# Kernel optimization log

Measured on AMD Instinct MI355X. Metric: run time of the kernel, lower is better.

The kernel has to match this reference:

```python
import jax, jax.numpy as jnp
import numpy as np


def phi(x):
    return jax.nn.elu(x) + 1.0


def setup_inputs() -> dict:
    key = jax.random.key(0)
    ks = jax.random.split(key, 6)
    B, C, H, W = 16, 256, 64, 64
    scale = 1.0 / np.sqrt(C)
    x = jax.random.normal(ks[0], (B, C, H, W), dtype=jnp.float32)
    Wq = jax.random.normal(ks[1], (C, C), dtype=jnp.float32) * scale
    Wk = jax.random.normal(ks[2], (C, C), dtype=jnp.float32) * scale
    Wv = jax.random.normal(ks[3], (C, C), dtype=jnp.float32) * scale
    Wo = jax.random.normal(ks[4], (C, C), dtype=jnp.float32) * scale
    bo = jnp.zeros((C,), dtype=jnp.float32)
    return {"x": x, "Wq": Wq, "Wk": Wk, "Wv": Wv, "Wo": Wo, "bo": bo}


def reference(x, Wq, Wk, Wv, Wo, bo):
    # 1x1 convs == channel matmuls: out[b,o,h,w] = sum_c W[o,c] x[b,c,h,w]
    q = jnp.einsum('oc,bchw->bohw', Wq, x)
    k = jnp.einsum('oc,bchw->bohw', Wk, x)
    v = jnp.einsum('oc,bchw->bohw', Wv, x)
    phi_q, phi_k, phi_v = phi(q), phi(k), phi(v)
    # context matrix per batch: [B, C, C]
    qv = jnp.einsum('bchw,bdhw->bcd', phi_q, phi_v)
    # per-batch 1x1 conv with weight qv[b] applied to phi_k[b]
    attended = jnp.einsum('bcd,bdhw->bchw', qv, phi_k)
    # output projection with bias; dropout is identity at eval
    out = jnp.einsum('oc,bchw->bohw', Wo, attended) + bo[None, :, None, None]
    return out
```

## Files before the change

### kernel.cpp

```cpp
#include <hip/hip_runtime.h>
#include <hip/hip_bf16.h>


typedef short  bf16x8 __attribute__((ext_vector_type(8)));
typedef float  f32x4  __attribute__((ext_vector_type(4)));
typedef unsigned short u16x4 __attribute__((ext_vector_type(4)));

#define NB 16
#define NC 256
#define NN 4096

__device__ __forceinline__ unsigned short f2bf(float f) {
    union { float f; unsigned u; } v; v.f = f;
    unsigned r = v.u + 0x7FFFu + ((v.u >> 16) & 1u);
    return (unsigned short)(r >> 16);
}

__device__ __forceinline__ float phi_act(float v) {
    return v > 0.f ? v + 1.f : __expf(v);
}

__device__ __forceinline__ void gemm128_nt(
    const unsigned short* __restrict__ A, int lda,
    const unsigned short* __restrict__ BT, int ldb,
    int k0, int nk, f32x4 (&acc)[4][4])
{
    __shared__ bf16x8 lsA[1032];
    __shared__ bf16x8 lsB[1032];
    const int t    = threadIdx.x;
    const int lane = t & 63;
    const int sr   = t >> 2;
    const int ss   = (t & 3) * 2;
    const int w    = t >> 6;
    const int wr   = (w >> 1) * 64;
    const int wc   = (w & 1) * 64;
    const int q    = lane >> 4;
    const int c15  = lane & 15;

    for (int kt = 0; kt < nk; ++kt) {
        const int kb = k0 + kt * 64;
        bf16x8 ra[4], rb[4];
        #pragma unroll
        for (int j = 0; j < 2; ++j) {
            const int r = sr + 64 * j;
            const bf16x8* ga = (const bf16x8*)(A + (size_t)r * lda + kb) + ss;
            ra[2 * j]     = ga[0];
            ra[2 * j + 1] = ga[1];
            const bf16x8* gb = (const bf16x8*)(BT + (size_t)r * ldb + kb) + ss;
            rb[2 * j]     = gb[0];
            rb[2 * j + 1] = gb[1];
        }
        if (kt) __syncthreads();
        #pragma unroll
        for (int j = 0; j < 2; ++j) {
            const int r = sr + 64 * j;
            lsA[(ss    ) * 129 + r] = ra[2 * j];
            lsA[(ss + 1) * 129 + r] = ra[2 * j + 1];
            lsB[(ss    ) * 129 + r] = rb[2 * j];
            lsB[(ss + 1) * 129 + r] = rb[2 * j + 1];
        }
        __syncthreads();
        #pragma unroll
        for (int g = 0; g < 2; ++g) {
            const int sb = (g * 4 + q) * 129;
            bf16x8 af[4], bfr[4];
            #pragma unroll
            for (int m = 0; m < 4; ++m) af[m]  = lsA[sb + wr + m * 16 + c15];
            #pragma unroll
            for (int n = 0; n < 4; ++n) bfr[n] = lsB[sb + wc + n * 16 + c15];
            #pragma unroll
            for (int m = 0; m < 4; ++m)
                #pragma unroll
                for (int n = 0; n < 4; ++n)
                    acc[m][n] = __builtin_amdgcn_mfma_f32_16x16x32_bf16(
                        af[m], bfr[n], acc[m][n], 0, 0, 0);
        }
    }
}

__global__ __launch_bounds__(256) void k_wconv(
    const float* __restrict__ Wq, const float* __restrict__ Wk,
    const float* __restrict__ Wv, const float* __restrict__ Wo,
    unsigned short* __restrict__ Wqkv, unsigned short* __restrict__ Wob)
{
    int i = blockIdx.x * 256 + threadIdx.x;
    if      (i < 65536)  Wqkv[i] = f2bf(Wq[i]);
    else if (i < 131072) Wqkv[i] = f2bf(Wk[i - 65536]);
    else if (i < 196608) Wqkv[i] = f2bf(Wv[i - 131072]);
    else if (i < 262144) Wob[i - 196608] = f2bf(Wo[i - 196608]);
}

__global__ __launch_bounds__(256) void k_xpose(
    const float* __restrict__ x, unsigned short* __restrict__ xT)
{
    __shared__ float tile[32][33];
    const int b  = blockIdx.z;
    const int n0 = blockIdx.x * 32, c0 = blockIdx.y * 32;
    const int tx = threadIdx.x, ty = threadIdx.y;
    const float* xp = x + ((size_t)b * NC + c0) * NN + n0;
    #pragma unroll
    for (int j = 0; j < 4; ++j)
        tile[ty + 8 * j][tx] = xp[(size_t)(ty + 8 * j) * NN + tx];
    __syncthreads();
    unsigned short* op = xT + ((size_t)b * NN + n0) * NC + c0;
    #pragma unroll
    for (int j = 0; j < 4; ++j)
        op[(size_t)(ty + 8 * j) * NC + tx] = f2bf(tile[tx][ty + 8 * j]);
}

__global__ __launch_bounds__(256) void k_proj(
    const unsigned short* __restrict__ Wqkv, const unsigned short* __restrict__ xT,
    unsigned short* __restrict__ phiQ, unsigned short* __restrict__ phiKT,
    unsigned short* __restrict__ phiV)
{
    const int bid = blockIdx.x;
    const int nt  = bid & 31;
    const int mt  = (bid >> 5) % 6;
    const int b   = bid / 192;
    const unsigned short* A  = Wqkv + mt * 128 * NC;
    const unsigned short* BT = xT + ((size_t)b * NN + nt * 128) * NC;
    f32x4 acc[4][4] = {};
    gemm128_nt(A, NC, BT, NC, 0, 4, acc);

    const int lane = threadIdx.x & 63;
    const int w    = threadIdx.x >> 6;
    const int wr   = (w >> 1) * 64, wc = (w & 1) * 64;
    const int q4   = (lane >> 4) * 4, c15 = lane & 15;
    const int p    = mt >> 1;
    const int rp0  = (mt & 1) * 128 + wr + q4;
    const int cb   = nt * 128 + wc + c15;
    if (p == 1) {
        unsigned short* dst = phiKT + (size_t)b * NN * NC;
        #pragma unroll
        for (int m = 0; m < 4; ++m)
            #pragma unroll
            for (int n = 0; n < 4; ++n) {
                u16x4 pk;
                #pragma unroll
                for (int i = 0; i < 4; ++i) pk[i] = f2bf(phi_act(acc[m][n][i]));
                *(u16x4*)(dst + (size_t)(cb + n * 16) * NC + rp0 + m * 16) = pk;
            }
    } else {
        unsigned short* dst = (p == 0 ? phiQ : phiV) + (size_t)b * NC * NN;
        #pragma unroll
        for (int m = 0; m < 4; ++m)
            #pragma unroll
            for (int i = 0; i < 4; ++i) {
                unsigned short* rowp = dst + (size_t)(rp0 + m * 16 + i) * NN + cb;
                #pragma unroll
                for (int n = 0; n < 4; ++n)
                    rowp[n * 16] = f2bf(phi_act(acc[m][n][i]));
            }
    }
}

__global__ __launch_bounds__(256) void k_qv(
    const unsigned short* __restrict__ phiQ, const unsigned short* __restrict__ phiV,
    float* __restrict__ qvTp)
{
    const int bid = blockIdx.x;
    const int s = bid & 3, nt = (bid >> 2) & 1, mt = (bid >> 3) & 1, b = bid >> 4;
    const unsigned short* A  = phiQ + ((size_t)b * NC + mt * 128) * NN;
    const unsigned short* BT = phiV + ((size_t)b * NC + nt * 128) * NN;
    f32x4 acc[4][4] = {};
    gemm128_nt(A, NN, BT, NN, s * 1024, 16, acc);

    const int lane = threadIdx.x & 63, w = threadIdx.x >> 6;
    const int wr = (w >> 1) * 64, wc = (w & 1) * 64;
    const int q4 = (lane >> 4) * 4, c15 = lane & 15;
    float* dst = qvTp + (((size_t)s * NB + b) << 16);
    const int c0 = mt * 128 + wr + q4;
    const int d0 = nt * 128 + wc + c15;
    #pragma unroll
    for (int m = 0; m < 4; ++m)
        #pragma unroll
        for (int n = 0; n < 4; ++n)
            *(f32x4*)(dst + (size_t)(d0 + n * 16) * NC + c0 + m * 16) = acc[m][n];
}

__global__ __launch_bounds__(256) void k_qvred(
    const float* __restrict__ p, unsigned short* __restrict__ qvT)
{
    const size_t i = (size_t)blockIdx.x * 256 + threadIdx.x;
    const f32x4* pv = (const f32x4*)p;
    f32x4 v = pv[i];
    v = v + pv[i + 262144];
    v = v + pv[i + 2 * 262144];
    v = v + pv[i + 3 * 262144];
    u16x4 o;
    #pragma unroll
    for (int j = 0; j < 4; ++j) o[j] = f2bf(v[j]);
    ((u16x4*)qvT)[i] = o;
}

__global__ __launch_bounds__(256) void k_mproj(
    const unsigned short* __restrict__ Wob, const unsigned short* __restrict__ qvT,
    unsigned short* __restrict__ Mb)
{
    const int bid = blockIdx.x;
    const int nt = bid & 1, mt = (bid >> 1) & 1, b = bid >> 2;
    const unsigned short* A  = Wob + mt * 128 * NC;
    const unsigned short* BT = qvT + ((size_t)b << 16) + nt * 128 * NC;
    f32x4 acc[4][4] = {};
    gemm128_nt(A, NC, BT, NC, 0, 4, acc);

    const int lane = threadIdx.x & 63, w = threadIdx.x >> 6;
    const int wr = (w >> 1) * 64, wc = (w & 1) * 64;
    const int q4 = (lane >> 4) * 4, c15 = lane & 15;
    unsigned short* dst = Mb + ((size_t)b << 16);
    const int o0 = mt * 128 + wr + q4;
    const int d0 = nt * 128 + wc + c15;
    #pragma unroll
    for (int m = 0; m < 4; ++m)
        #pragma unroll
        for (int i = 0; i < 4; ++i) {
            const int row = o0 + m * 16 + i;
            #pragma unroll
            for (int n = 0; n < 4; ++n)
                dst[(size_t)row * NC + d0 + n * 16] = f2bf(acc[m][n][i]);
        }
}

__global__ __launch_bounds__(256) void k_out(
    const unsigned short* __restrict__ Mb, const unsigned short* __restrict__ phiKT,
    const float* __restrict__ bo, float* __restrict__ out)
{
    const int bid = blockIdx.x;
    const int nt = bid & 31, mt = (bid >> 5) & 1, b = bid >> 6;
    const unsigned short* A  = Mb + ((size_t)b << 16) + mt * 128 * NC;
    const unsigned short* BT = phiKT + (size_t)b * NN * NC + (size_t)nt * 128 * NC;
    f32x4 acc[4][4] = {};
    gemm128_nt(A, NC, BT, NC, 0, 4, acc);

    const int lane = threadIdx.x & 63, w = threadIdx.x >> 6;
    const int wr = (w >> 1) * 64, wc = (w & 1) * 64;
    const int q4 = (lane >> 4) * 4, c15 = lane & 15;
    float* dst = out + (size_t)b * NC * NN;
    const int o0 = mt * 128 + wr + q4;
    const int n0 = nt * 128 + wc + c15;
    #pragma unroll
    for (int m = 0; m < 4; ++m)
        #pragma unroll
        for (int i = 0; i < 4; ++i) {
            const int row  = o0 + m * 16 + i;
            const float bb = bo[row];
            #pragma unroll
            for (int n = 0; n < 4; ++n)
                dst[(size_t)row * NN + n0 + n * 16] = acc[m][n][i] + bb;
        }
}

extern "C" void kernel_launch(void* const* d_in, const int* in_sizes, int n_in,
                              void* d_out, int out_size, void* d_ws, size_t ws_size,
                              hipStream_t stream)
{
    (void)in_sizes; (void)n_in; (void)out_size; (void)ws_size;
    const float* x  = (const float*)d_in[0];
    const float* Wq = (const float*)d_in[1];
    const float* Wk = (const float*)d_in[2];
    const float* Wv = (const float*)d_in[3];
    const float* Wo = (const float*)d_in[4];
    const float* bo = (const float*)d_in[5];
    float* out = (float*)d_out;

    char* ws = (char*)d_ws;
    size_t off = 0;
    auto alloc = [&](size_t bytes) {
        void* p = ws + off;
        off += (bytes + 255) & ~(size_t)255;
        return p;
    };
    unsigned short* xT    = (unsigned short*)alloc((size_t)NB * NN * NC * 2);
    unsigned short* phiQ  = (unsigned short*)alloc((size_t)NB * NC * NN * 2);
    unsigned short* phiV  = (unsigned short*)alloc((size_t)NB * NC * NN * 2);
    unsigned short* phiKT = (unsigned short*)alloc((size_t)NB * NN * NC * 2);
    float*          qvTp  = (float*)alloc((size_t)4 * NB * NC * NC * 4);
    unsigned short* qvT   = (unsigned short*)alloc((size_t)NB * NC * NC * 2);
    unsigned short* Mb    = (unsigned short*)alloc((size_t)NB * NC * NC * 2);
    unsigned short* Wqkv  = (unsigned short*)alloc((size_t)768 * NC * 2);
    unsigned short* Wob   = (unsigned short*)alloc((size_t)NC * NC * 2);

    k_wconv<<<1024, 256, 0, stream>>>(Wq, Wk, Wv, Wo, Wqkv, Wob);
    k_xpose<<<dim3(NN / 32, NC / 32, NB), dim3(32, 8), 0, stream>>>(x, xT);
    k_proj<<<NB * 6 * 32, 256, 0, stream>>>(Wqkv, xT, phiQ, phiKT, phiV);
    k_qv<<<NB * 2 * 2 * 4, 256, 0, stream>>>(phiQ, phiV, qvTp);
    k_qvred<<<1024, 256, 0, stream>>>(qvTp, qvT);
    k_mproj<<<NB * 2 * 2, 256, 0, stream>>>(Wob, qvT, Mb);
    k_out<<<NB * 2 * 32, 256, 0, stream>>>(Mb, phiKT, bo, out);
}
```

Measured before the change: 137.2 us.

## Use direct global-to-LDS loads with swizzle, vectorize stores and transpose, split qv more

Replaces the register-staged LDS fill in the shared GEMM with global_load_lds direct copies into an XOR-swizzled layout. It adds a template option to swap the MFMA operands so epilogues can write contiguous vectorized rows, and widens the transpose kernel to 64x64 tiles with float4 loads. It also doubles the split-K factor in the qv kernel to 8 partials and reuses the xT buffer for the partial sums. Together these target the scalar, uncoalesced stores and the LDS staging overhead, at the cost of more reduction traffic and a dependence on xT being dead by the time qv runs.

```diff
diff --git a/kernel.cpp b/kernel.cpp
--- a/kernel.cpp
+++ b/kernel.cpp
@@ -20,60 +20,64 @@
     return v > 0.f ? v + 1.f : __expf(v);
 }
 
-__device__ __forceinline__ void gemm128_nt(
+__device__ __forceinline__ void gload_lds16(const void* g, void* l) {
+    __builtin_amdgcn_global_load_lds(
+        (const __attribute__((address_space(1))) void*)g,
+        (__attribute__((address_space(3))) void*)l, 16, 0, 0);
+}
+
+__device__ __forceinline__ void stage_tile(
+    const unsigned short* __restrict__ src, int ld, int kb, char* lds, int t)
+{
+    const int kslot  = t & 7;
+    const int rbase  = t >> 3;
+    const int srcOff = (kslot * 16) ^ ((rbase & 7) << 4);
+    const int wbase  = (t >> 6) * 1024;
+    #pragma unroll
+    for (int i = 0; i < 4; ++i) {
+        const int r = i * 32 + rbase;
+        const char* g = (const char*)(src + (size_t)r * ld + kb) + srcOff;
+        gload_lds16(g, lds + i * 4096 + wbase);
+    }
+}
+
+__device__ __forceinline__ bf16x8 frag_ld(const char* lds, int row, int kbyte) {
+    return *(const bf16x8*)(lds + row * 128 + (kbyte ^ ((row & 7) << 4)));
+}
+
+template<bool SWAP>
+__device__ __forceinline__ void gemm128(
     const unsigned short* __restrict__ A, int lda,
     const unsigned short* __restrict__ BT, int ldb,
-    int k0, int nk, f32x4 (&acc)[4][4])
-{
-    __shared__ bf16x8 lsA[1032];
-    __shared__ bf16x8 lsB[1032];
-    const int t    = threadIdx.x;
+    int k0, int nk, char* lsA, char* lsB, f32x4 (&acc)[4][4])
+{
+    const int t = threadIdx.x;
     const int lane = t & 63;
-    const int sr   = t >> 2;
-    const int ss   = (t & 3) * 2;
-    const int w    = t >> 6;
-    const int wr   = (w >> 1) * 64;
-    const int wc   = (w & 1) * 64;
-    const int q    = lane >> 4;
-    const int c15  = lane & 15;
+    const int w  = t >> 6;
+    const int wr = (w >> 1) * 64, wc = (w & 1) * 64;
+    const int q  = lane >> 4, c15 = lane & 15;
 
     for (int kt = 0; kt < nk; ++kt) {
         const int kb = k0 + kt * 64;
-        bf16x8 ra[4], rb[4];
-        #pragma unroll
-        for (int j = 0; j < 2; ++j) {
-            const int r = sr + 64 * j;
-            const bf16x8* ga = (const bf16x8*)(A + (size_t)r * lda + kb) + ss;
-            ra[2 * j]     = ga[0];
-            ra[2 * j + 1] = ga[1];
-            const bf16x8* gb = (const bf16x8*)(BT + (size_t)r * ldb + kb) + ss;
-            rb[2 * j]     = gb[0];
-            rb[2 * j + 1] = gb[1];
-        }
         if (kt) __syncthreads();
-        #pragma unroll
-        for (int j = 0; j < 2; ++j) {
-            const int r = sr + 64 * j;
-            lsA[(ss    ) * 129 + r] = ra[2 * j];
-            lsA[(ss + 1) * 129 + r] = ra[2 * j + 1];
-            lsB[(ss    ) * 129 + r] = rb[2 * j];
-            lsB[(ss + 1) * 129 + r] = rb[2 * j + 1];
-        }
+        stage_tile(A,  lda, kb, lsA, t);
+        stage_tile(BT, ldb, kb, lsB, t);
         __syncthreads();
         #pragma unroll
         for (int g = 0; g < 2; ++g) {
-            const int sb = (g * 4 + q) * 129;
+            const int kbyte = g * 64 + q * 16;
             bf16x8 af[4], bfr[4];
             #pragma unroll
-            for (int m = 0; m < 4; ++m) af[m]  = lsA[sb + wr + m * 16 + c15];
-            #pragma unroll
-            for (int n = 0; n < 4; ++n) bfr[n] = lsB[sb + wc + n * 16 + c15];
+            for (int m = 0; m < 4; ++m) af[m]  = frag_ld(lsA, wr + m * 16 + c15, kbyte);
+            #pragma unroll
+            for (int n = 0; n < 4; ++n) bfr[n] = frag_ld(lsB, wc + n * 16 + c15, kbyte);
             #pragma unroll
             for (int m = 0; m < 4; ++m)
                 #pragma unroll
                 for (int n = 0; n < 4; ++n)
-                    acc[m][n] = __builtin_amdgcn_mfma_f32_16x16x32_bf16(
-                        af[m], bfr[n], acc[m][n], 0, 0, 0);
+                    acc[m][n] = SWAP
+                        ? __builtin_amdgcn_mfma_f32_16x16x32_bf16(bfr[n], af[m], acc[m][n], 0, 0, 0)
+                        : __builtin_amdgcn_mfma_f32_16x16x32_bf16(af[m], bfr[n], acc[m][n], 0, 0, 0);
         }
     }
 }
@@ -93,19 +97,29 @@
 __global__ __launch_bounds__(256) void k_xpose(
     const float* __restrict__ x, unsigned short* __restrict__ xT)
 {
-    __shared__ float tile[32][33];
+    __shared__ float tile[64][68];
     const int b  = blockIdx.z;
-    const int n0 = blockIdx.x * 32, c0 = blockIdx.y * 32;
-    const int tx = threadIdx.x, ty = threadIdx.y;
+    const int n0 = blockIdx.x * 64, c0 = blockIdx.y * 64;
+    const int t  = threadIdx.x;
     const float* xp = x + ((size_t)b * NC + c0) * NN + n0;
-    #pragma unroll
-    for (int j = 0; j < 4; ++j)
-        tile[ty + 8 * j][tx] = xp[(size_t)(ty + 8 * j) * NN + tx];
+    const int cc = t >> 4, nq = t & 15;
+    #pragma unroll
+    for (int j = 0; j < 4; ++j) {
+        const int c = j * 16 + cc;
+        f32x4 v = *(const f32x4*)(xp + (size_t)c * NN + nq * 4);
+        *(f32x4*)&tile[c][nq * 4] = v;
+    }
     __syncthreads();
     unsigned short* op = xT + ((size_t)b * NN + n0) * NC + c0;
-    #pragma unroll
-    for (int j = 0; j < 4; ++j)
-        op[(size_t)(ty + 8 * j) * NC + tx] = f2bf(tile[tx][ty + 8 * j]);
+    const int nn0 = t >> 4, cq = t & 15;
+    #pragma unroll
+    for (int j = 0; j < 4; ++j) {
+        const int nn = j * 16 + nn0;
+        u16x4 o;
+        #pragma unroll
+        for (int ii = 0; ii < 4; ++ii) o[ii] = f2bf(tile[cq * 4 + ii][nn]);
+        *(u16x4*)(op + (size_t)nn * NC + cq * 4) = o;
+    }
 }
 
 __global__ __launch_bounds__(256) void k_proj(
@@ -113,24 +127,26 @@
     unsigned short* __restrict__ phiQ, unsigned short* __restrict__ phiKT,
     unsigned short* __restrict__ phiV)
 {
+    __shared__ char lds[32768];
     const int bid = blockIdx.x;
     const int nt  = bid & 31;
     const int mt  = (bid >> 5) % 6;
     const int b   = bid / 192;
     const unsigned short* A  = Wqkv + mt * 128 * NC;
     const unsigned short* BT = xT + ((size_t)b * NN + nt * 128) * NC;
-    f32x4 acc[4][4] = {};
-    gemm128_nt(A, NC, BT, NC, 0, 4, acc);
 
     const int lane = threadIdx.x & 63;
     const int w    = threadIdx.x >> 6;
     const int wr   = (w >> 1) * 64, wc = (w & 1) * 64;
     const int q4   = (lane >> 4) * 4, c15 = lane & 15;
     const int p    = mt >> 1;
-    const int rp0  = (mt & 1) * 128 + wr + q4;
-    const int cb   = nt * 128 + wc + c15;
+
+    f32x4 acc[4][4] = {};
     if (p == 1) {
+        gemm128<false>(A, NC, BT, NC, 0, 4, lds, lds + 16384, acc);
         unsigned short* dst = phiKT + (size_t)b * NN * NC;
+        const int cb = (mt & 1) * 128 + wr + q4;
+        const int nb = nt * 128 + wc + c15;
         #pragma unroll
         for (int m = 0; m < 4; ++m)
             #pragma unroll
@@ -138,18 +154,21 @@
                 u16x4 pk;
                 #pragma unroll
                 for (int i = 0; i < 4; ++i) pk[i] = f2bf(phi_act(acc[m][n][i]));
-                *(u16x4*)(dst + (size_t)(cb + n * 16) * NC + rp0 + m * 16) = pk;
+                *(u16x4*)(dst + (size_t)(nb + n * 16) * NC + cb + m * 16) = pk;
             }
     } else {
+        gemm128<true>(A, NC, BT, NC, 0, 4, lds, lds + 16384, acc);
         unsigned short* dst = (p == 0 ? phiQ : phiV) + (size_t)b * NC * NN;
+        const int ob = (mt & 1) * 128 + wr + c15;
+        const int nb = nt * 128 + wc + q4;
         #pragma unroll
         for (int m = 0; m < 4; ++m)
             #pragma unroll
-            for (int i = 0; i < 4; ++i) {
-                unsigned short* rowp = dst + (size_t)(rp0 + m * 16 + i) * NN + cb;
+            for (int n = 0; n < 4; ++n) {
+                u16x4 pk;
                 #pragma unroll
-                for (int n = 0; n < 4; ++n)
-                    rowp[n * 16] = f2bf(phi_act(acc[m][n][i]));
+                for (int i = 0; i < 4; ++i) pk[i] = f2bf(phi_act(acc[m][n][i]));
+                *(u16x4*)(dst + (size_t)(ob + m * 16) * NN + nb + n * 16) = pk;
             }
     }
 }
@@ -158,12 +177,13 @@
     const unsigned short* __restrict__ phiQ, const unsigned short* __restrict__ phiV,
     float* __restrict__ qvTp)
 {
+    __shared__ char lds[32768];
     const int bid = blockIdx.x;
-    const int s = bid & 3, nt = (bid >> 2) & 1, mt = (bid >> 3) & 1, b = bid >> 4;
+    const int s = bid & 7, nt = (bid >> 3) & 1, mt = (bid >> 4) & 1, b = bid >> 5;
     const unsigned short* A  = phiQ + ((size_t)b * NC + mt * 128) * NN;
     const unsigned short* BT = phiV + ((size_t)b * NC + nt * 128) * NN;
     f32x4 acc[4][4] = {};
-    gemm128_nt(A, NN, BT, NN, s * 1024, 16, acc);
+    gemm128<false>(A, NN, BT, NN, s * 512, 8, lds, lds + 16384, acc);
 
     const int lane = threadIdx.x & 63, w = threadIdx.x >> 6;
     const int wr = (w >> 1) * 64, wc = (w & 1) * 64;
@@ -184,9 +204,8 @@
     const size_t i = (size_t)blockIdx.x * 256 + threadIdx.x;
     const f32x4* pv = (const f32x4*)p;
     f32x4 v = pv[i];
-    v = v + pv[i + 262144];
-    v = v + pv[i + 2 * 262144];
-    v = v + pv[i + 3 * 262144];
+    #pragma unroll
+    for (int s = 1; s < 8; ++s) v = v + pv[i + (size_t)s * 262144];
     u16x4 o;
     #pragma unroll
     for (int j = 0; j < 4; ++j) o[j] = f2bf(v[j]);
@@ -197,27 +216,28 @@
     const unsigned short* __restrict__ Wob, const unsigned short* __restrict__ qvT,
     unsigned short* __restrict__ Mb)
 {
+    __shared__ char lds[32768];
     const int bid = blockIdx.x;
     const int nt = bid & 1, mt = (bid >> 1) & 1, b = bid >> 2;
     const unsigned short* A  = Wob + mt * 128 * NC;
     const unsigned short* BT = qvT + ((size_t)b << 16) + nt * 128 * NC;
     f32x4 acc[4][4] = {};
-    gemm128_nt(A, NC, BT, NC, 0, 4, acc);
+    gemm128<true>(A, NC, BT, NC, 0, 4, lds, lds + 16384, acc);
 
     const int lane = threadIdx.x & 63, w = threadIdx.x >> 6;
     const int wr = (w >> 1) * 64, wc = (w & 1) * 64;
     const int q4 = (lane >> 4) * 4, c15 = lane & 15;
     unsigned short* dst = Mb + ((size_t)b << 16);
-    const int o0 = mt * 128 + wr + q4;
-    const int d0 = nt * 128 + wc + c15;
+    const int ob = mt * 128 + wr + c15;
+    const int db = nt * 128 + wc + q4;
     #pragma unroll
     for (int m = 0; m < 4; ++m)
         #pragma unroll
-        for (int i = 0; i < 4; ++i) {
-            const int row = o0 + m * 16 + i;
-            #pragma unroll
-            for (int n = 0; n < 4; ++n)
-                dst[(size_t)row * NC + d0 + n * 16] = f2bf(acc[m][n][i]);
+        for (int n = 0; n < 4; ++n) {
+            u16x4 pk;
+            #pragma unroll
+            for (int i = 0; i < 4; ++i) pk[i] = f2bf(acc[m][n][i]);
+            *(u16x4*)(dst + (size_t)(ob + m * 16) * NC + db + n * 16) = pk;
         }
 }
 
@@ -225,29 +245,30 @@
     const unsigned short* __restrict__ Mb, const unsigned short* __restrict__ phiKT,
     const float* __restrict__ bo, float* __restrict__ out)
 {
+    __shared__ char lds[32768];
     const int bid = blockIdx.x;
     const int nt = bid & 31, mt = (bid >> 5) & 1, b = bid >> 6;
     const unsigned short* A  = Mb + ((size_t)b << 16) + mt * 128 * NC;
     const unsigned short* BT = phiKT + (size_t)b * NN * NC + (size_t)nt * 128 * NC;
     f32x4 acc[4][4] = {};
-    gemm128_nt(A, NC, BT, NC, 0, 4, acc);
+    gemm128<true>(A, NC, BT, NC, 0, 4, lds, lds + 16384, acc);
 
     const int lane = threadIdx.x & 63, w = threadIdx.x >> 6;
     const int wr = (w >> 1) * 64, wc = (w & 1) * 64;
     const int q4 = (lane >> 4) * 4, c15 = lane & 15;
     float* dst = out + (size_t)b * NC * NN;
-    const int o0 = mt * 128 + wr + q4;
-    const int n0 = nt * 128 + wc + c15;
-    #pragma unroll
-    for (int m = 0; m < 4; ++m)
-        #pragma unroll
-        for (int i = 0; i < 4; ++i) {
-            const int row  = o0 + m * 16 + i;
-            const float bb = bo[row];
-            #pragma unroll
-            for (int n = 0; n < 4; ++n)
-                dst[(size_t)row * NN + n0 + n * 16] = acc[m][n][i] + bb;
+    #pragma unroll
+    for (int m = 0; m < 4; ++m) {
+        const int o  = mt * 128 + wr + m * 16 + c15;
+        const float bb = bo[o];
+        #pragma unroll
+        for (int n = 0; n < 4; ++n) {
+            f32x4 v = acc[m][n];
+            #pragma unroll
+            for (int i = 0; i < 4; ++i) v[i] += bb;
+            *(f32x4*)(dst + (size_t)o * NN + nt * 128 + wc + n * 16 + q4) = v;
         }
+    }
 }
 
 extern "C" void kernel_launch(void* const* d_in, const int* in_sizes, int n_in,
@@ -274,16 +295,16 @@
     unsigned short* phiQ  = (unsigned short*)alloc((size_t)NB * NC * NN * 2);
     unsigned short* phiV  = (unsigned short*)alloc((size_t)NB * NC * NN * 2);
     unsigned short* phiKT = (unsigned short*)alloc((size_t)NB * NN * NC * 2);
-    float*          qvTp  = (float*)alloc((size_t)4 * NB * NC * NC * 4);
     unsigned short* qvT   = (unsigned short*)alloc((size_t)NB * NC * NC * 2);
     unsigned short* Mb    = (unsigned short*)alloc((size_t)NB * NC * NC * 2);
     unsigned short* Wqkv  = (unsigned short*)alloc((size_t)768 * NC * 2);
     unsigned short* Wob   = (unsigned short*)alloc((size_t)NC * NC * 2);
+    float* qvTp = (float*)xT;
 
     k_wconv<<<1024, 256, 0, stream>>>(Wq, Wk, Wv, Wo, Wqkv, Wob);
-    k_xpose<<<dim3(NN / 32, NC / 32, NB), dim3(32, 8), 0, stream>>>(x, xT);
+    k_xpose<<<dim3(NN / 64, NC / 64, NB), dim3(256), 0, stream>>>(x, xT);
     k_proj<<<NB * 6 * 32, 256, 0, stream>>>(Wqkv, xT, phiQ, phiKT, phiV);
-    k_qv<<<NB * 2 * 2 * 4, 256, 0, stream>>>(phiQ, phiV, qvTp);
+    k_qv<<<NB * 2 * 2 * 8, 256, 0, stream>>>(phiQ, phiV, qvTp);
     k_qvred<<<1024, 256, 0, stream>>>(qvTp, qvT);
     k_mproj<<<NB * 2 * 2, 256, 0, stream>>>(Wob, qvT, Mb);
     k_out<<<NB * 2 * 32, 256, 0, stream>>>(Mb, phiKT, bo, out);
```

Result: faster. 126.4 us (-7.9%).
